# Kernel tuning notes

Measured on AMD Instinct MI355X. Metric: run time of the kernel, lower is better.

## Reference

```python
import jax, jax.numpy as jnp
import numpy as np

EPS_W = 1e-9


def area2d(a, b, c):
    # signed parallelogram area; a/b/c are [..., >=2] points
    return (b[..., 0] - a[..., 0]) * (c[..., 1] - a[..., 1]) - (b[..., 1] - a[..., 1]) * (c[..., 0] - a[..., 0])


def lookup_table(size):
    # square table of 2d points (x, y) in [-1, 1], matching torch meshgrid('ij') + rot90
    lin = jnp.linspace(-1.0, 1.0, size, dtype=jnp.float32)
    xx, yy = jnp.meshgrid(lin, lin, indexing='ij')
    t = jnp.stack([xx, yy], axis=-1)
    return jnp.rot90(t, 1, axes=(0, 1))  # [S,S,2]


def grid_sample_bilinear(img, grid):
    # img [C,H,W]; grid [...,2] with (x,y) in [-1,1]; bilinear, zero padding, align_corners=True
    C, H, W = img.shape
    x, y = grid[..., 0], grid[..., 1]
    ix = (x + 1.0) * (W - 1) * 0.5
    iy = (y + 1.0) * (H - 1) * 0.5
    ix0 = jnp.floor(ix)
    iy0 = jnp.floor(iy)
    ix1 = ix0 + 1.0
    iy1 = iy0 + 1.0
    wx1 = ix - ix0
    wx0 = 1.0 - wx1
    wy1 = iy - iy0
    wy0 = 1.0 - wy1

    def tap(iyf, ixf):
        inb = (ixf >= 0) & (ixf <= W - 1) & (iyf >= 0) & (iyf <= H - 1)
        ii = jnp.clip(ixf, 0, W - 1).astype(jnp.int32)
        jj = jnp.clip(iyf, 0, H - 1).astype(jnp.int32)
        return img[:, jj, ii] * inb.astype(img.dtype)  # [C, ...]

    return (tap(iy0, ix0) * (wy0 * wx0) + tap(iy0, ix1) * (wy0 * wx1)
            + tap(iy1, ix0) * (wy1 * wx0) + tap(iy1, ix1) * (wy1 * wx1))


def _render(vertices, uv, uvmap, faces, uvfaces, size):
    pts = lookup_table(size)              # [S,S,2]
    uvn = uv * 2.0 - 1.0                  # uv scaled to [-1,1] as in __init__
    tris = vertices[faces]                # [K,3,3]
    uvt = uvn[uvfaces]                    # [K,3,2]

    # backface cull mask (z-component of cross(v1-v0, v2-v0) > 0)
    e1 = tris[:, 1] - tris[:, 0]
    e2 = tris[:, 2] - tris[:, 0]
    normal_z = e1[:, 0] * e2[:, 1] - e1[:, 1] * e2[:, 0]
    valid = normal_z > 0

    zinit = jnp.min(vertices, axis=0)[-1]
    result0 = jnp.zeros((4, size, size), jnp.float32)
    zbuf0 = jnp.full((size, size), zinit, dtype=jnp.float32)

    def step(carry, xs):
        result, zbuf = carry
        tri, uvtri, ok = xs               # tri [3,3], uvtri [3,2], ok scalar bool
        tri2d = tri[:, :2]
        w = area2d(tri2d[0], tri2d[1], tri2d[2])
        # sub areas against every pixel (dense equivalent of AABB + inside masks)
        pAB = area2d(tri2d[1], pts, tri2d[0])   # [S,S]
        pCB = area2d(tri2d[2], pts, tri2d[1])
        pCA = area2d(tri2d[0], pts, tri2d[2])
        inside = (pAB > 0) & (pCB > 0) & (pCA > 0)
        ws = jnp.where(w >= EPS_W, w, 1.0)      # safe divide; masked out below
        w1 = pCB / ws
        w2 = pCA / ws
        w3 = 1.0 - w1 - w2
        z = w1 * tri[0, 2] + w2 * tri[1, 2] + w3 * tri[2, 2]   # [S,S]
        mask = ok & (w >= EPS_W) & inside & (z >= zbuf)
        # barycentric uv interpolation + bilinear texture lookup
        ptsUV = w1[..., None] * uvtri[0] + w2[..., None] * uvtri[1] + w3[..., None] * uvtri[2]  # [S,S,2]
        rgb = grid_sample_bilinear(uvmap, ptsUV)  # [3,S,S]
        zbuf = jnp.where(mask, z, zbuf)
        rgba = jnp.concatenate([rgb, jnp.ones((1, size, size), result.dtype)], axis=0)
        result = jnp.where(mask[None], rgba, result)
        return (result, zbuf), None

    (result, _), _ = jax.lax.scan(step, (result0, zbuf0), (tris, uvt, valid))
    return result


def setup_inputs() -> dict:
    key = jax.random.key(0)
    k0, k1, k2, k3, k4 = jax.random.split(key, 5)
    V, K, M, T, S = 1500, 1500, 2000, 1024, 512
    vertices = jax.random.normal(k0, (V, 3), dtype=jnp.float32)
    faces = jax.random.randint(k1, (K, 3), 0, V)
    uv = jax.random.uniform(k2, (M, 2), dtype=jnp.float32)
    uvfaces = jax.random.randint(k3, (K, 3), 0, M)
    uvmap = jax.random.normal(k4, (3, T, T), dtype=jnp.float32)
    return {"vertices": vertices, "faces": faces, "uv": uv,
            "uvfaces": uvfaces, "uvmap": uvmap, "size": S}


def reference(vertices, faces, uv, uvfaces, uvmap, size):
    return _render(vertices, uv, uvmap, faces, uvfaces, size)
```

## Files before the change

kernel.cpp:

```cpp
#include <hip/hip_runtime.h>
#include <hip/hip_fp16.h>
#include <cmath>

#pragma clang fp contract(off)

#define MAXK 2048
#define BATCH 256

struct TriUV {
  float u0x, u0y, u1x, u1y;
  float u2x, u2y, pad0, pad1;
};

__device__ __forceinline__ float h2f(unsigned v) {
  __half_raw r; r.x = (unsigned short)v;
  return __half2float(__half(r));
}
__device__ __forceinline__ unsigned f2h(float v) {
  return (unsigned)__half_as_ushort(__float2half(v));
}
__device__ __forceinline__ unsigned pkh(float lo, float hi) {
  return f2h(lo) | (f2h(hi) << 16);
}
__device__ __forceinline__ unsigned fmapu(float f) {
  unsigned b = __float_as_uint(f);
  return (b & 0x80000000u) ? ~b : (b | 0x80000000u);
}
__device__ __forceinline__ float funmap(unsigned m) {
  return __uint_as_float((m & 0x80000000u) ? (m ^ 0x80000000u) : ~m);
}

__device__ __forceinline__ float lin_at(int i, int n) {
#pragma clang fp contract(off)
  if (i == n - 1) return 1.0f;
  float step = (float)i / (float)(n - 1);
  return (-1.0f) * (1.0f - step) + 1.0f * step;
}

__global__ __launch_bounds__(256) void prep_kernel(
    const float* __restrict__ verts, const int* __restrict__ faces,
    const float* __restrict__ uv, const int* __restrict__ uvfaces, int V, int K,
    float4* __restrict__ q0S, float4* __restrict__ q1S,
    float4* __restrict__ q2S, float4* __restrict__ q3S,
    float4* __restrict__ bboxS, uint4* __restrict__ apS,
    float4* __restrict__ metaS, float4* __restrict__ planeS,
    TriUV* __restrict__ tuv, float* __restrict__ zinit) {
#pragma clang fp contract(off)
  __shared__ float smz[256];
  int tid = (int)threadIdx.x;
  int bid = (int)blockIdx.x;
  if (bid == 0) {
    float m = 3.402823466e38f;
    for (int i = tid; i < V; i += 256) m = fminf(m, verts[3 * i + 2]);
    smz[tid] = m;
    __syncthreads();
    for (int s2 = 128; s2 > 0; s2 >>= 1) {
      if (tid < s2) smz[tid] = fminf(smz[tid], smz[tid + s2]);
      __syncthreads();
    }
    if (tid == 0) *zinit = smz[0];
    return;
  }
  int t = (bid - 1) * 256 + tid;
  if (t >= K) return;
  int i0 = faces[3 * t + 0], i1 = faces[3 * t + 1], i2 = faces[3 * t + 2];
  float t0x = verts[3 * i0 + 0], t0y = verts[3 * i0 + 1], z0 = verts[3 * i0 + 2];
  float t1x = verts[3 * i1 + 0], t1y = verts[3 * i1 + 1], z1 = verts[3 * i1 + 2];
  float t2x = verts[3 * i2 + 0], t2y = verts[3 * i2 + 1], z2 = verts[3 * i2 + 2];
  int j0 = uvfaces[3 * t + 0], j1 = uvfaces[3 * t + 1], j2 = uvfaces[3 * t + 2];
  TriUV u;
  u.u0x = uv[2 * j0 + 0] * 2.0f - 1.0f;
  u.u0y = uv[2 * j0 + 1] * 2.0f - 1.0f;
  u.u1x = uv[2 * j1 + 0] * 2.0f - 1.0f;
  u.u1y = uv[2 * j1 + 1] * 2.0f - 1.0f;
  u.u2x = uv[2 * j2 + 0] * 2.0f - 1.0f;
  u.u2y = uv[2 * j2 + 1] * 2.0f - 1.0f;
  u.pad0 = 0.0f; u.pad1 = 0.0f;
  tuv[t] = u;
  float w = (t1x - t0x) * (t2y - t0y) - (t1y - t0y) * (t2x - t0x);
  if (w < 1e-9f) {
    bboxS[t] = make_float4(3.0e38f, -3.0e38f, 3.0e38f, -3.0e38f);
    return;
  }
  float dAy = t0y - t1y, dAx = t0x - t1x;
  float dBy = t1y - t2y, dBx = t1x - t2x;
  float dCy = t2y - t0y, dCx = t2x - t0x;
  q0S[t] = make_float4(t1x, t1y, dAy, dAx);
  q1S[t] = make_float4(t2x, t2y, dBy, dBx);
  q2S[t] = make_float4(t0x, t0y, dCy, dCx);
  q3S[t] = make_float4(z0, z1, z2, w);
  bboxS[t] = make_float4(fminf(fminf(t0x, t1x), t2x),
                         fmaxf(fmaxf(t0x, t1x), t2x),
                         fminf(fminf(t0y, t1y), t2y),
                         fmaxf(fmaxf(t0y, t1y), t2y));
  float fA = t1y * dAx - t1x * dAy;
  float fB = t2y * dBx - t2x * dBy;
  float fC = t0y * dCx - t0x * dCy;
  float sA = fabsf(dAy) + fabsf(dAx) + fabsf(fA);
  float sB = fabsf(dBy) + fabsf(dBx) + fabsf(fB);
  float sC = fabsf(dCy) + fabsf(dCx) + fabsf(fC);
  float M = fmaxf(fmaxf(sA, sB), sC) * 9.766e-4f + 1e-4f;
  apS[t] = make_uint4(pkh(dAy, dAx), pkh(fA, dBy), pkh(dBx, fB),
                      pkh(dCy, dCx));
  metaS[t] = make_float4(M, fC, __int_as_float(t), 0.0f);
  float zmx = fmaxf(fmaxf(z0, z1), z2);
  float gatef = zmx + 1e-3f + 1e-4f / w;
  float gx = (z0 * dBy + z1 * dCy + z2 * dAy) / w;
  float gy = -(z0 * dBx + z1 * dCx + z2 * dAx) / w;
  float cc = (z0 * fB + z1 * fC + z2 * fA) / w;
  float mm = (fabsf(z0 * fB) + fabsf(z1 * fC) + fabsf(z2 * fA) +
              fabsf(z0 * dBy) + fabsf(z1 * dCy) + fabsf(z2 * dAy) +
              fabsf(z0 * dBx) + fabsf(z1 * dCx) + fabsf(z2 * dAx)) *
                 (2e-6f / w) +
             1e-3f + 1e-4f / w + 1e-4f;
  planeS[t] = make_float4(gx, gy, cc + mm, gatef);
}

__global__ __launch_bounds__(1024) void render_kernel(
    const float4* __restrict__ q0S, const float4* __restrict__ q1S,
    const float4* __restrict__ q2S, const float4* __restrict__ q3S,
    const float4* __restrict__ bboxS, const uint4* __restrict__ apS,
    const float4* __restrict__ metaS, const float4* __restrict__ planeS,
    int N, const TriUV* __restrict__ tuv, const float* __restrict__ zinitp,
    const float* __restrict__ uvmap, int T, float* __restrict__ out, int S) {
#pragma clang fp contract(off)
  __shared__ unsigned short s_kept[MAXK];
  __shared__ unsigned s_tgm[MAXK];
  __shared__ unsigned s_em[MAXK];
  __shared__ unsigned long long s_key[256];
  __shared__ unsigned s_zu[256];
  __shared__ unsigned s_hist[256];
  __shared__ int s_cur[256];
  __shared__ unsigned s_wsum[4];
  __shared__ uint4 s_ap[BATCH];
  __shared__ float4 s_mt[BATCH];
  __shared__ float4 s_q0[BATCH];
  __shared__ float4 s_q1[BATCH];
  __shared__ float4 s_q2[BATCH];
  __shared__ float4 s_q3[BATCH];

  int tid = (int)threadIdx.x;
  int wv = tid >> 6, ln = tid & 63;
  int s = wv >> 2, q = wv & 3;
  int pix = (q << 6) + ln;
  int tilesX = S >> 4;
  int tileX = (int)blockIdx.x % tilesX;
  int tileY = (int)blockIdx.x / tilesX;
  int j = (tileX << 4) + (pix & 15);
  int i = (tileY << 4) + (pix >> 4);
  float px = lin_at(j, S);
  float py = lin_at(S - 1 - i, S);
  float pxlo = lin_at(tileX << 4, S);
  float pxhi = lin_at((tileX << 4) + 15, S);
  float pylo = lin_at(S - 1 - ((tileY << 4) + 15), S);
  float pyhi = lin_at(S - 1 - (tileY << 4), S);

  float zinit = *zinitp;
  unsigned zinit_m = fmapu(zinit);
  if (tid < 256) {
    s_zu[tid] = zinit_m;
    s_key[tid] = ((unsigned long long)zinit_m << 32);
    s_hist[tid] = 0u;
  }
  volatile unsigned* vzu = s_zu;
  __syncthreads();

  bool kA = false, kB = false;
  int bA = 0, bB = 0;
  unsigned gA = 0, gB = 0;
  {
    int t = tid;
    if (t < N) {
      float4 bb = bboxS[t];
      if (bb.x <= pxhi && bb.y >= pxlo && bb.z <= pyhi && bb.w >= pylo) {
        float4 pl = planeS[t];
        float ub = pl.z + fmaxf(pl.x * pxlo, pl.x * pxhi) +
                   fmaxf(pl.y * pylo, pl.y * pyhi);
        float tg = fminf(pl.w, ub);
        kA = true;
        bA = min(max((int)((4.0f - tg) * 32.0f), 0), 255);
        gA = fmapu(tg);
      }
    }
    t = tid + 1024;
    if (t < N) {
      float4 bb = bboxS[t];
      if (bb.x <= pxhi && bb.y >= pxlo && bb.z <= pyhi && bb.w >= pylo) {
        float4 pl = planeS[t];
        float ub = pl.z + fmaxf(pl.x * pxlo, pl.x * pxhi) +
                   fmaxf(pl.y * pylo, pl.y * pyhi);
        float tg = fminf(pl.w, ub);
        kB = true;
        bB = min(max((int)((4.0f - tg) * 32.0f), 0), 255);
        gB = fmapu(tg);
      }
    }
  }
  if (kA) atomicAdd(&s_hist[bA], 1u);
  if (kB) atomicAdd(&s_hist[bB], 1u);
  __syncthreads();
  unsigned hx = 0, hinc = 0;
  if (tid < 256) {
    hx = s_hist[tid];
    unsigned v = hx;
#pragma unroll
    for (int d = 1; d < 64; d <<= 1) {
      unsigned tv = __shfl_up(v, d, 64);
      if (ln >= d) v += tv;
    }
    if (ln == 63) s_wsum[wv] = v;
    hinc = v;
  }
  __syncthreads();
  if (tid < 256) {
    unsigned add = 0;
    for (int w2 = 0; w2 < wv; ++w2) add += s_wsum[w2];
    hinc += add;
    s_hist[tid] = hinc;
    s_cur[tid] = (int)(hinc - hx);
  }
  __syncthreads();
  int nk = (int)s_hist[255];
  if (kA) {
    int sl = atomicAdd(&s_cur[bA], 1);
    s_kept[sl] = (unsigned short)tid;
    s_tgm[sl] = gA;
    float ef = (bA == 0) ? 3.402823466e38f : (4.0f - (float)bA * 0.03125f);
    s_em[sl] = fmapu(ef);
  }
  if (kB) {
    int sl = atomicAdd(&s_cur[bB], 1);
    s_kept[sl] = (unsigned short)(tid + 1024);
    s_tgm[sl] = gB;
    float ef = (bB == 0) ? 3.402823466e38f : (4.0f - (float)bB * 0.03125f);
    s_em[sl] = fmapu(ef);
  }
  __syncthreads();

  for (int base = 0; base < nk; base += BATCH) {
    __syncthreads();
    {
      int u = tid & (BATCH - 1);
      int tslot = base + u;
      if (tslot < nk) {
        int idx = s_kept[tslot];
        int sel = tid >> 8;
        if (sel == 0) s_ap[u] = apS[idx];
        else if (sel == 1) s_mt[u] = metaS[idx];
        else if (sel == 2) s_q3[u] = q3S[idx];
        else s_q0[u] = q0S[idx];
        if (tid < 512) {
          if (sel == 0) s_q1[u] = q1S[idx];
          else s_q2[u] = q2S[idx];
        }
      }
    }
    __syncthreads();
    int nb = min(BATCH, nk - base);
    for (int k = s; k < nb; k += 4) {
      int a = base + k;
      unsigned em = s_em[a];
      unsigned zb = vzu[pix];
      if (__all(em < zb)) break;
      if (em >= zb && s_tgm[a] >= zb) {
        uint4 ap = s_ap[k];
        float M = s_mt[k].x, fC = s_mt[k].y;
        float aA = fmaf(px, h2f(ap.x & 0xffffu),
                        fmaf(-py, h2f(ap.x >> 16), h2f(ap.y & 0xffffu)));
        float aB = fmaf(px, h2f(ap.y >> 16),
                        fmaf(-py, h2f(ap.z & 0xffffu), h2f(ap.z >> 16)));
        float aC = fmaf(px, h2f(ap.w & 0xffffu),
                        fmaf(-py, h2f(ap.w >> 16), fC));
        if (fminf(fminf(aA, aB), aC) > -M) {
          float4 q0 = s_q0[k], q1 = s_q1[k], q2 = s_q2[k];
          float pAB = (px - q0.x) * q0.z - (py - q0.y) * q0.w;
          float pCB = (px - q1.x) * q1.z - (py - q1.y) * q1.w;
          float pCA = (px - q2.x) * q2.z - (py - q2.y) * q2.w;
          if (pAB > 0.0f && pCB > 0.0f && pCA > 0.0f) {
            float4 q3 = s_q3[k];
            float w = q3.w;
            float bzf = funmap(vzu[pix]);
            float zs = (pCB * q3.x + pCA * q3.y) + ((w - pCB) - pCA) * q3.z;
            if (w < 1e-3f || zs >= (bzf - 1e-3f) * w) {
              float w1 = pCB / w;
              float w2 = pCA / w;
              float w3 = (1.0f - w1) - w2;
              float z = (w1 * q3.x + w2 * q3.y) + w3 * q3.z;
              int o = __float_as_int(s_mt[k].z);
              unsigned zm = fmapu(z);
              unsigned long long key =
                  ((unsigned long long)zm << 32) | (unsigned)(o + 1);
              atomicMax(&s_key[pix], key);
              atomicMax(&s_zu[pix], zm);
            }
          }
        }
      }
    }
    int nxt = base + BATCH;
    bool done;
    if (nxt >= nk) done = true;
    else done = (s_em[nxt] < vzu[pix]);
    if (__syncthreads_and((int)done)) break;
  }
  __syncthreads();

  if (tid < 256) {
    unsigned long long key = s_key[tid];
    unsigned oP1 = (unsigned)(key & 0xFFFFFFFFULL);
    float o0 = 0.0f, o1 = 0.0f, o2 = 0.0f, o3 = 0.0f;
    if (oP1 != 0) {
      int o = (int)oP1 - 1;
      float4 q1 = q1S[o], q2 = q2S[o], q3 = q3S[o];
      float pCB = (px - q1.x) * q1.z - (py - q1.y) * q1.w;
      float pCA = (px - q2.x) * q2.z - (py - q2.y) * q2.w;
      float w1 = pCB / q3.w;
      float w2 = pCA / q3.w;
      float w3 = (1.0f - w1) - w2;
      TriUV u = tuv[o];
      float x = (w1 * u.u0x + w2 * u.u1x) + w3 * u.u2x;
      float y = (w1 * u.u0y + w2 * u.u1y) + w3 * u.u2y;
      float WH = (float)(T - 1);
      float fx = ((x + 1.0f) * WH) * 0.5f;
      float fy = ((y + 1.0f) * WH) * 0.5f;
      float ix0 = floorf(fx), iy0 = floorf(fy);
      float ix1 = ix0 + 1.0f, iy1 = iy0 + 1.0f;
      float wx1 = fx - ix0, wx0 = 1.0f - wx1;
      float wy1 = fy - iy0, wy0 = 1.0f - wy1;
      float w00 = wy0 * wx0, w01 = wy0 * wx1;
      float w10 = wy1 * wx0, w11 = wy1 * wx1;
      bool bx0 = (ix0 >= 0.0f) && (ix0 <= WH);
      bool bx1 = (ix1 >= 0.0f) && (ix1 <= WH);
      bool by0 = (iy0 >= 0.0f) && (iy0 <= WH);
      bool by1 = (iy1 >= 0.0f) && (iy1 <= WH);
      float m00 = (by0 && bx0) ? 1.0f : 0.0f;
      float m01 = (by0 && bx1) ? 1.0f : 0.0f;
      float m10 = (by1 && bx0) ? 1.0f : 0.0f;
      float m11 = (by1 && bx1) ? 1.0f : 0.0f;
      int cx0 = (int)fminf(fmaxf(ix0, 0.0f), WH);
      int cx1 = (int)fminf(fmaxf(ix1, 0.0f), WH);
      int cy0 = (int)fminf(fmaxf(iy0, 0.0f), WH);
      int cy1 = (int)fminf(fmaxf(iy1, 0.0f), WH);
      int TT = T * T;
      int i00 = cy0 * T + cx0, i01 = cy0 * T + cx1;
      int i10 = cy1 * T + cx0, i11 = cy1 * T + cx1;
      {
        const float* img = uvmap;
        float v00 = img[i00] * m00, v01 = img[i01] * m01;
        float v10 = img[i10] * m10, v11 = img[i11] * m11;
        o0 = ((v00 * w00 + v01 * w01) + v10 * w10) + v11 * w11;
      }
      {
        const float* img = uvmap + TT;
        float v00 = img[i00] * m00, v01 = img[i01] * m01;
        float v10 = img[i10] * m10, v11 = img[i11] * m11;
        o1 = ((v00 * w00 + v01 * w01) + v10 * w10) + v11 * w11;
      }
      {
        const float* img = uvmap + 2 * TT;
        float v00 = img[i00] * m00, v01 = img[i01] * m01;
        float v10 = img[i10] * m10, v11 = img[i11] * m11;
        o2 = ((v00 * w00 + v01 * w01) + v10 * w10) + v11 * w11;
      }
      o3 = 1.0f;
    }
    int p = i * S + j;
    int SS = S * S;
    out[p] = o0;
    out[SS + p] = o1;
    out[2 * SS + p] = o2;
    out[3 * SS + p] = o3;
  }
}

extern "C" void kernel_launch(void* const* d_in, const int* in_sizes, int n_in,
                              void* d_out, int out_size, void* d_ws,
                              size_t ws_size, hipStream_t stream) {
  const float* verts = (const float*)d_in[0];
  const int* faces = (const int*)d_in[1];
  const float* uv = (const float*)d_in[2];
  const int* uvfaces = (const int*)d_in[3];
  const float* uvmap = (const float*)d_in[4];
  int V = in_sizes[0] / 3;
  int K = in_sizes[1] / 3;
  int T = (int)lroundf(sqrtf((float)(in_sizes[4] / 3)));
  int S = (int)lroundf(sqrtf((float)(out_size / 4)));
  float* outp = (float*)d_out;

  char* ws = (char*)d_ws;
  size_t off = 0;
  auto alloc = [&](size_t bytes) {
    void* p = ws + off;
    off = (off + bytes + 255) & ~(size_t)255;
    return p;
  };
  float* zinit = (float*)alloc(4);
  float4* q0S = (float4*)alloc((size_t)MAXK * 16);
  float4* q1S = (float4*)alloc((size_t)MAXK * 16);
  float4* q2S = (float4*)alloc((size_t)MAXK * 16);
  float4* q3S = (float4*)alloc((size_t)MAXK * 16);
  float4* bboxS = (float4*)alloc((size_t)MAXK * 16);
  uint4* apS = (uint4*)alloc((size_t)MAXK * 16);
  float4* metaS = (float4*)alloc((size_t)MAXK * 16);
  float4* planeS = (float4*)alloc((size_t)MAXK * 16);
  TriUV* tuv = (TriUV*)alloc((size_t)K * sizeof(TriUV));

  int pblocks = 1 + (K + 255) / 256;
  prep_kernel<<<pblocks, 256, 0, stream>>>(verts, faces, uv, uvfaces, V, K,
                                           q0S, q1S, q2S, q3S, bboxS, apS,
                                           metaS, planeS, tuv, zinit);
  int tiles = (S >> 4) * (S >> 4);
  render_kernel<<<tiles, 1024, 0, stream>>>(q0S, q1S, q2S, q3S, bboxS, apS,
                                            metaS, planeS, K, tuv, zinit,
                                            uvmap, T, outp, S);
}
```

Before: 32.18 us.

## Read triangle data directly from global memory instead of batched LDS staging

Removes the per-batch cooperative staging of triangle records into shared memory, along with its barriers and the batch-level early-exit check. Each wave now loops over all kept triangles and loads the records it needs straight from global memory (typically cached, since all waves read the same indices). This drops the __syncthreads overhead and the loads of triangles that are never tested. In exchange, every tested triangle costs a scattered global load with higher latency than LDS.

```diff
diff --git a/kernel.cpp b/kernel.cpp
--- a/kernel.cpp
+++ b/kernel.cpp
@@ -5,7 +5,6 @@
 #pragma clang fp contract(off)
 
 #define MAXK 2048
-#define BATCH 256
 
 struct TriUV {
   float u0x, u0y, u1x, u1y;
@@ -132,12 +131,6 @@
   __shared__ unsigned s_hist[256];
   __shared__ int s_cur[256];
   __shared__ unsigned s_wsum[4];
-  __shared__ uint4 s_ap[BATCH];
-  __shared__ float4 s_mt[BATCH];
-  __shared__ float4 s_q0[BATCH];
-  __shared__ float4 s_q1[BATCH];
-  __shared__ float4 s_q2[BATCH];
-  __shared__ float4 s_q3[BATCH];
 
   int tid = (int)threadIdx.x;
   int wv = tid >> 6, ln = tid & 63;
@@ -237,71 +230,46 @@
   }
   __syncthreads();
 
-  for (int base = 0; base < nk; base += BATCH) {
-    __syncthreads();
-    {
-      int u = tid & (BATCH - 1);
-      int tslot = base + u;
-      if (tslot < nk) {
-        int idx = s_kept[tslot];
-        int sel = tid >> 8;
-        if (sel == 0) s_ap[u] = apS[idx];
-        else if (sel == 1) s_mt[u] = metaS[idx];
-        else if (sel == 2) s_q3[u] = q3S[idx];
-        else s_q0[u] = q0S[idx];
-        if (tid < 512) {
-          if (sel == 0) s_q1[u] = q1S[idx];
-          else s_q2[u] = q2S[idx];
-        }
-      }
-    }
-    __syncthreads();
-    int nb = min(BATCH, nk - base);
-    for (int k = s; k < nb; k += 4) {
-      int a = base + k;
-      unsigned em = s_em[a];
-      unsigned zb = vzu[pix];
-      if (__all(em < zb)) break;
-      if (em >= zb && s_tgm[a] >= zb) {
-        uint4 ap = s_ap[k];
-        float M = s_mt[k].x, fC = s_mt[k].y;
-        float aA = fmaf(px, h2f(ap.x & 0xffffu),
-                        fmaf(-py, h2f(ap.x >> 16), h2f(ap.y & 0xffffu)));
-        float aB = fmaf(px, h2f(ap.y >> 16),
-                        fmaf(-py, h2f(ap.z & 0xffffu), h2f(ap.z >> 16)));
-        float aC = fmaf(px, h2f(ap.w & 0xffffu),
-                        fmaf(-py, h2f(ap.w >> 16), fC));
-        if (fminf(fminf(aA, aB), aC) > -M) {
-          float4 q0 = s_q0[k], q1 = s_q1[k], q2 = s_q2[k];
-          float pAB = (px - q0.x) * q0.z - (py - q0.y) * q0.w;
-          float pCB = (px - q1.x) * q1.z - (py - q1.y) * q1.w;
-          float pCA = (px - q2.x) * q2.z - (py - q2.y) * q2.w;
-          if (pAB > 0.0f && pCB > 0.0f && pCA > 0.0f) {
-            float4 q3 = s_q3[k];
-            float w = q3.w;
-            float bzf = funmap(vzu[pix]);
-            float zs = (pCB * q3.x + pCA * q3.y) + ((w - pCB) - pCA) * q3.z;
-            if (w < 1e-3f || zs >= (bzf - 1e-3f) * w) {
-              float w1 = pCB / w;
-              float w2 = pCA / w;
-              float w3 = (1.0f - w1) - w2;
-              float z = (w1 * q3.x + w2 * q3.y) + w3 * q3.z;
-              int o = __float_as_int(s_mt[k].z);
-              unsigned zm = fmapu(z);
-              unsigned long long key =
-                  ((unsigned long long)zm << 32) | (unsigned)(o + 1);
-              atomicMax(&s_key[pix], key);
-              atomicMax(&s_zu[pix], zm);
-            }
+  for (int a = s; a < nk; a += 4) {
+    unsigned em = s_em[a];
+    unsigned zb = vzu[pix];
+    if (__all(em < zb)) break;
+    if (em >= zb && s_tgm[a] >= zb) {
+      int idx = s_kept[a];
+      uint4 ap = apS[idx];
+      float4 mt = metaS[idx];
+      float M = mt.x, fC = mt.y;
+      float aA = fmaf(px, h2f(ap.x & 0xffffu),
+                      fmaf(-py, h2f(ap.x >> 16), h2f(ap.y & 0xffffu)));
+      float aB = fmaf(px, h2f(ap.y >> 16),
+                      fmaf(-py, h2f(ap.z & 0xffffu), h2f(ap.z >> 16)));
+      float aC = fmaf(px, h2f(ap.w & 0xffffu),
+                      fmaf(-py, h2f(ap.w >> 16), fC));
+      if (fminf(fminf(aA, aB), aC) > -M) {
+        float4 q0 = q0S[idx], q1 = q1S[idx], q2 = q2S[idx];
+        float pAB = (px - q0.x) * q0.z - (py - q0.y) * q0.w;
+        float pCB = (px - q1.x) * q1.z - (py - q1.y) * q1.w;
+        float pCA = (px - q2.x) * q2.z - (py - q2.y) * q2.w;
+        if (pAB > 0.0f && pCB > 0.0f && pCA > 0.0f) {
+          float4 q3 = q3S[idx];
+          float w = q3.w;
+          float bzf = funmap(vzu[pix]);
+          float zs = (pCB * q3.x + pCA * q3.y) + ((w - pCB) - pCA) * q3.z;
+          if (w < 1e-3f || zs >= (bzf - 1e-3f) * w) {
+            float w1 = pCB / w;
+            float w2 = pCA / w;
+            float w3 = (1.0f - w1) - w2;
+            float z = (w1 * q3.x + w2 * q3.y) + w3 * q3.z;
+            int o = __float_as_int(mt.z);
+            unsigned zm = fmapu(z);
+            unsigned long long key =
+                ((unsigned long long)zm << 32) | (unsigned)(o + 1);
+            atomicMax(&s_key[pix], key);
+            atomicMax(&s_zu[pix], zm);
           }
         }
       }
     }
-    int nxt = base + BATCH;
-    bool done;
-    if (nxt >= nk) done = true;
-    else done = (s_em[nxt] < vzu[pix]);
-    if (__syncthreads_and((int)done)) break;
   }
   __syncthreads();
 
```

New measurement: 32.57 us. Within noise of the previous version (+1.2%).
